# Optimization experiments

Measured on AMD Instinct MI355X. Metric: run time of the kernel, lower is better.

The kernel has to match this reference:

```python
import jax, jax.numpy as jnp
import numpy as np

GROUPS = 8
EPS = 1e-5
NUM_HEADS = 8


def group_norm(x, gamma, beta):
    # x: [B, C, N]; GroupNorm over (C//G, N) per group, per sample (torch semantics)
    B, C, N = x.shape
    xg = x.reshape(B, GROUPS, (C // GROUPS) * N)
    mean = xg.mean(axis=-1, keepdims=True)
    var = xg.var(axis=-1, keepdims=True)
    xn = ((xg - mean) * jax.lax.rsqrt(var + EPS)).reshape(B, C, N)
    return xn * gamma[None, :, None] + beta[None, :, None]


def setup_inputs() -> dict:
    key = jax.random.key(0)
    ks = jax.random.split(key, 6)
    B, N, C = 4, 2048, 512
    s = 0.02
    return {
        "x": jax.random.normal(ks[0], (B, N, C), jnp.float32),
        "pe": jax.random.normal(ks[1], (B, N, C), jnp.float32),
        "qkv_w": jax.random.normal(ks[2], (3 * C, C), jnp.float32) * s,
        "proj_w": jax.random.normal(ks[3], (C, C), jnp.float32) * s,
        "proj_b": jnp.zeros((C,), jnp.float32),
        "conv1_w": jax.random.normal(ks[4], (C, C), jnp.float32) * s,
        "conv1_b": jnp.zeros((C,), jnp.float32),
        "gn1_g": jnp.ones((C,), jnp.float32),
        "gn1_b": jnp.zeros((C,), jnp.float32),
        "conv2_w": jax.random.normal(ks[5], (C, C), jnp.float32) * s,
        "conv2_b": jnp.zeros((C,), jnp.float32),
        "gn2_g": jnp.ones((C,), jnp.float32),
        "gn2_b": jnp.zeros((C,), jnp.float32),
    }


def reference(x, pe, qkv_w, proj_w, proj_b, conv1_w, conv1_b, gn1_g, gn1_b,
              conv2_w, conv2_b, gn2_g, gn2_b):
    B, N, C = x.shape
    H = NUM_HEADS
    D = C // H
    scale = D ** -0.5

    pe_t = pe.transpose(0, 2, 1)  # [B, C, N]
    # Conv1d(kernel=1) == per-position linear over channels
    p1 = group_norm(jnp.einsum('oc,bcn->bon', conv1_w, pe_t) + conv1_b[None, :, None], gn1_g, gn1_b)
    p2 = group_norm(jnp.einsum('oc,bcn->bon', conv2_w, pe_t) + conv2_b[None, :, None], gn2_g, gn2_b)
    pe_1 = p1.transpose(0, 2, 1)                 # [B, N, C]
    pe_attn = jax.nn.sigmoid(jnp.einsum('bnc,bcm->bnm', pe_1, p2))  # [B, N, N]

    qkv = (x @ qkv_w.T).reshape(B, N, 3, H, D).transpose(2, 0, 3, 1, 4)  # [3, B, H, N, D]
    q, k, v = qkv[0], qkv[1], qkv[2]

    attn = jnp.einsum('bhnd,bhmd->bhnm', q, k) * scale
    attn = attn * pe_attn[:, None, :, :]
    attn = jax.nn.softmax(attn, axis=-1)

    out = jnp.einsum('bhnm,bhmd->bhnd', attn, v)          # [B, H, N, D]
    out = out.transpose(0, 2, 1, 3).reshape(B, N, C)
    return out @ proj_w.T + proj_b
```

## Files before the change

### kernel.cpp

```cpp
#include <hip/hip_runtime.h>
#include <hip/hip_bf16.h>

typedef __attribute__((ext_vector_type(8))) short bf16x8;
typedef __attribute__((ext_vector_type(4))) float f32x4;

__device__ __forceinline__ float bfu2f(unsigned int u) {
    return __uint_as_float(u << 16);
}
__device__ __forceinline__ unsigned short f2bfu(float f) {
    unsigned int u = __float_as_uint(f);
    u += 0x7fffu + ((u >> 16) & 1u);
    return (unsigned short)(u >> 16);
}

__global__ __launch_bounds__(256) void cvt2(const float* __restrict__ s0, unsigned short* __restrict__ d0,
                                            const float* __restrict__ s1, unsigned short* __restrict__ d1) {
    int i = blockIdx.x * 256 + threadIdx.x;
    const int stride = gridDim.x * 256;
    for (; i < 1048576; i += stride) {
        float4 v = reinterpret_cast<const float4*>(s0)[i];
        ushort4 o;
        o.x = f2bfu(v.x); o.y = f2bfu(v.y); o.z = f2bfu(v.z); o.w = f2bfu(v.w);
        reinterpret_cast<ushort4*>(d0)[i] = o;
        float4 u = reinterpret_cast<const float4*>(s1)[i];
        ushort4 p;
        p.x = f2bfu(u.x); p.y = f2bfu(u.y); p.z = f2bfu(u.z); p.w = f2bfu(u.w);
        reinterpret_cast<ushort4*>(d1)[i] = p;
    }
}

__global__ __launch_bounds__(256) void cvtw(const float* __restrict__ s0, unsigned short* __restrict__ d0,
                                            const float* __restrict__ s1, unsigned short* __restrict__ d1,
                                            const float* __restrict__ s2, unsigned short* __restrict__ d2,
                                            const float* __restrict__ s3, unsigned short* __restrict__ d3) {
    int i = blockIdx.x * 256 + threadIdx.x;
    const int stride = gridDim.x * 256;
    for (; i < 393216; i += stride) {
        const float* s; unsigned short* d; int j;
        if (i < 196608)      { s = s0; d = d0; j = i; }
        else if (i < 262144) { s = s1; d = d1; j = i - 196608; }
        else if (i < 327680) { s = s2; d = d2; j = i - 262144; }
        else                 { s = s3; d = d3; j = i - 327680; }
        float4 v = reinterpret_cast<const float4*>(s)[j];
        ushort4 o;
        o.x = f2bfu(v.x); o.y = f2bfu(v.y); o.z = f2bfu(v.z); o.w = f2bfu(v.w);
        reinterpret_cast<ushort4*>(d)[j] = o;
    }
}

template <int EPI>
__global__ __launch_bounds__(256) void gemm_nt(
    const unsigned short* __restrict__ A, const unsigned short* __restrict__ B,
    void* __restrict__ C0, void* __restrict__ C1, void* __restrict__ C2,
    const float* __restrict__ bias, int K, long sA, long sB, long sC) {
    __shared__ unsigned short As[128 * 40];
    __shared__ unsigned short Bs[128 * 40];
    const int tid = threadIdx.x;
    const int l = tid & 63, w = tid >> 6;
    const int wr = w >> 1, wc = w & 1, lr = l & 15, lh = l >> 4;
    const int m0 = blockIdx.y * 128, n0 = blockIdx.x * 128;
    A += (size_t)blockIdx.z * sA;
    B += (size_t)blockIdx.z * sB;
    f32x4 acc[4][4] = {};
    const int rowS = tid >> 2, partS = tid & 3;

    for (int k0 = 0; k0 < K; k0 += 32) {
        *reinterpret_cast<uint4*>(&As[rowS * 40 + partS * 8]) =
            *reinterpret_cast<const uint4*>(A + (size_t)(m0 + rowS) * K + k0 + partS * 8);
        *reinterpret_cast<uint4*>(&As[(rowS + 64) * 40 + partS * 8]) =
            *reinterpret_cast<const uint4*>(A + (size_t)(m0 + rowS + 64) * K + k0 + partS * 8);
        *reinterpret_cast<uint4*>(&Bs[rowS * 40 + partS * 8]) =
            *reinterpret_cast<const uint4*>(B + (size_t)(n0 + rowS) * K + k0 + partS * 8);
        *reinterpret_cast<uint4*>(&Bs[(rowS + 64) * 40 + partS * 8]) =
            *reinterpret_cast<const uint4*>(B + (size_t)(n0 + rowS + 64) * K + k0 + partS * 8);
        __syncthreads();
        bf16x8 af[4], bfr[4];
#pragma unroll
        for (int i = 0; i < 4; i++)
            af[i] = *reinterpret_cast<const bf16x8*>(&As[(wr * 64 + i * 16 + lr) * 40 + lh * 8]);
#pragma unroll
        for (int i = 0; i < 4; i++)
            bfr[i] = *reinterpret_cast<const bf16x8*>(&Bs[(wc * 64 + i * 16 + lr) * 40 + lh * 8]);
#pragma unroll
        for (int mi = 0; mi < 4; mi++)
#pragma unroll
            for (int ni = 0; ni < 4; ni++)
                acc[mi][ni] = __builtin_amdgcn_mfma_f32_16x16x32_bf16(af[mi], bfr[ni], acc[mi][ni], 0, 0, 0);
        __syncthreads();
    }

#pragma unroll
    for (int mi = 0; mi < 4; mi++) {
#pragma unroll
        for (int ni = 0; ni < 4; ni++) {
#pragma unroll
            for (int r = 0; r < 4; r++) {
                const int row = m0 + wr * 64 + mi * 16 + lh * 4 + r;
                const int col = n0 + wc * 64 + ni * 16 + lr;
                float v = acc[mi][ni][r];
                if constexpr (EPI == 0) {
                    v += bias[col];
                    ((unsigned short*)C0)[(size_t)row * 512 + col] = f2bfu(v);
                } else if constexpr (EPI == 1) {
                    const int part = col >> 9, hh = (col >> 6) & 7, d = col & 63;
                    const int b = row >> 11, n = row & 2047;
                    const size_t bh = (size_t)(b * 8 + hh);
                    if (part == 0)
                        ((unsigned short*)C0)[(bh * 2048 + n) * 64 + d] = f2bfu(v * 0.1803368801111244f);
                    else if (part == 1)
                        ((unsigned short*)C1)[(bh * 2048 + n) * 64 + d] = f2bfu(v);
                    else
                        ((unsigned short*)C2)[(bh * 64 + d) * 2048 + n] = f2bfu(v);
                } else if constexpr (EPI == 2) {
                    const float sg = 1.0f / (1.0f + __expf(-v));
                    ((unsigned short*)C0)[(size_t)blockIdx.z * sC + (size_t)row * 2048 + col] = f2bfu(sg);
                } else {
                    ((float*)C0)[(size_t)row * 512 + col] = v + bias[col];
                }
            }
        }
    }
}

__global__ __launch_bounds__(256) void gn_stats_part(const unsigned short* __restrict__ c1,
                                                     const unsigned short* __restrict__ c2,
                                                     float* __restrict__ part) {
    const int bgc = blockIdx.x;
    const int b = bgc >> 6, g = (bgc >> 3) & 7, ch = bgc & 7;
    const int tid = threadIdx.x;
    const size_t base = ((size_t)b * 2048 + ch * 256) * 512 + g * 64;
    float s1 = 0.f, q1 = 0.f, s2 = 0.f, q2 = 0.f;
    for (int c = tid; c < 2048; c += 256) {
        const int n = c >> 3, i8 = (c & 7) * 8;
        const size_t off = base + (size_t)n * 512 + i8;
        uint4 v1 = *reinterpret_cast<const uint4*>(c1 + off);
        uint4 v2 = *reinterpret_cast<const uint4*>(c2 + off);
        unsigned int a1[4] = {v1.x, v1.y, v1.z, v1.w};
        unsigned int a2[4] = {v2.x, v2.y, v2.z, v2.w};
#pragma unroll
        for (int j = 0; j < 4; j++) {
            float x0 = bfu2f(a1[j] & 0xffffu), x1 = bfu2f(a1[j] >> 16);
            s1 += x0 + x1; q1 += x0 * x0 + x1 * x1;
            float y0 = bfu2f(a2[j] & 0xffffu), y1 = bfu2f(a2[j] >> 16);
            s2 += y0 + y1; q2 += y0 * y0 + y1 * y1;
        }
    }
#pragma unroll
    for (int off = 32; off >= 1; off >>= 1) {
        s1 += __shfl_down(s1, off); q1 += __shfl_down(q1, off);
        s2 += __shfl_down(s2, off); q2 += __shfl_down(q2, off);
    }
    __shared__ float red[4][4];
    if ((tid & 63) == 0) {
        const int wv = tid >> 6;
        red[0][wv] = s1; red[1][wv] = q1; red[2][wv] = s2; red[3][wv] = q2;
    }
    __syncthreads();
    if (tid == 0) {
        part[bgc * 4 + 0] = red[0][0] + red[0][1] + red[0][2] + red[0][3];
        part[bgc * 4 + 1] = red[1][0] + red[1][1] + red[1][2] + red[1][3];
        part[bgc * 4 + 2] = red[2][0] + red[2][1] + red[2][2] + red[2][3];
        part[bgc * 4 + 3] = red[3][0] + red[3][1] + red[3][2] + red[3][3];
    }
}

__global__ __launch_bounds__(256) void gn_apply(unsigned short* __restrict__ c1,
                                                unsigned short* __restrict__ c2,
                                                const float* __restrict__ part,
                                                const float* __restrict__ g1, const float* __restrict__ b1,
                                                const float* __restrict__ g2, const float* __restrict__ b2) {
    __shared__ float sst[32][4];
    const int tid = threadIdx.x;
    if (tid < 32) {
        float S1 = 0.f, Q1 = 0.f, S2 = 0.f, Q2 = 0.f;
        for (int ch = 0; ch < 8; ch++) {
            const float* p = part + ((tid << 3) + ch) * 4;
            S1 += p[0]; Q1 += p[1]; S2 += p[2]; Q2 += p[3];
        }
        const float inv = 1.0f / 131072.0f;
        float m1 = S1 * inv, m2 = S2 * inv;
        float v1 = fmaxf(Q1 * inv - m1 * m1, 0.f);
        float v2 = fmaxf(Q2 * inv - m2 * m2, 0.f);
        sst[tid][0] = m1;
        sst[tid][1] = rsqrtf(v1 + 1e-5f);
        sst[tid][2] = m2;
        sst[tid][3] = rsqrtf(v2 + 1e-5f);
    }
    __syncthreads();
    int i = blockIdx.x * 256 + tid;
    const int stride = gridDim.x * 256;
    for (; i < 524288; i += stride) {
        const size_t e = (size_t)i * 8;
        const int b = (int)(e >> 20);
        const int o = (int)(e & 511);
        const int g = o >> 6;
        const float* st = sst[(b << 3) + g];
        const float m1 = st[0], r1 = st[1], m2 = st[2], r2 = st[3];
        uint4 v1 = *reinterpret_cast<const uint4*>(c1 + e);
        uint4 v2 = *reinterpret_cast<const uint4*>(c2 + e);
        unsigned int a1[4] = {v1.x, v1.y, v1.z, v1.w};
        unsigned int a2[4] = {v2.x, v2.y, v2.z, v2.w};
        unsigned int o1[4], o2[4];
#pragma unroll
        for (int j = 0; j < 4; j++) {
            const int oo = o + j * 2;
            float x0 = (bfu2f(a1[j] & 0xffffu) - m1) * r1 * g1[oo] + b1[oo];
            float x1 = (bfu2f(a1[j] >> 16) - m1) * r1 * g1[oo + 1] + b1[oo + 1];
            o1[j] = (unsigned int)f2bfu(x0) | ((unsigned int)f2bfu(x1) << 16);
            float y0 = (bfu2f(a2[j] & 0xffffu) - m2) * r2 * g2[oo] + b2[oo];
            float y1 = (bfu2f(a2[j] >> 16) - m2) * r2 * g2[oo + 1] + b2[oo + 1];
            o2[j] = (unsigned int)f2bfu(y0) | ((unsigned int)f2bfu(y1) << 16);
        }
        uint4 w1; w1.x = o1[0]; w1.y = o1[1]; w1.z = o1[2]; w1.w = o1[3];
        uint4 w2; w2.x = o2[0]; w2.y = o2[1]; w2.z = o2[2]; w2.w = o2[3];
        *reinterpret_cast<uint4*>(c1 + e) = w1;
        *reinterpret_cast<uint4*>(c2 + e) = w2;
    }
}

__global__ __launch_bounds__(256, 4) void attn_fused(
    const unsigned short* __restrict__ qb, const unsigned short* __restrict__ kb,
    const unsigned short* __restrict__ vT, const unsigned short* __restrict__ pea,
    unsigned short* __restrict__ hbuf) {
    __shared__ unsigned short Ks[2][64 * 64];
    __shared__ unsigned short Vs[2][64 * 64];
    const int tid = threadIdx.x, l = tid & 63, w = tid >> 6;
    const int lr = l & 15, lh = l >> 4;
    const int bid = blockIdx.x;
    const int h = bid >> 7, rst = bid & 127, nt = rst & 31, b = rst >> 5;
    const size_t bh = (size_t)(b * 8 + h);
    const unsigned short* qp = qb + bh * 2048 * 64;
    const unsigned short* kp = kb + bh * 2048 * 64;
    const unsigned short* vp = vT + bh * 64 * 2048;
    const unsigned short* pep = pea + (size_t)b * 2048 * 2048;
    const int n0 = nt * 64;

    bf16x8 qf[2];
    qf[0] = *reinterpret_cast<const bf16x8*>(qp + (size_t)(n0 + 16 * w + lr) * 64 + lh * 8);
    qf[1] = *reinterpret_cast<const bf16x8*>(qp + (size_t)(n0 + 16 * w + lr) * 64 + 32 + lh * 8);

    const int swz = (lr & 7) << 4;
    const int colK0 = ((16 * lh) ^ swz) >> 1;
    const int colK1 = ((64 + 16 * lh) ^ swz) >> 1;

    const unsigned short* perp = pep + (size_t)(n0 + 16 * w + lr) * 2048;
    uint2 peR[4];
#pragma unroll
    for (int mf = 0; mf < 4; mf++)
        peR[mf] = *reinterpret_cast<const uint2*>(perp + 16 * mf + 4 * lh);

    f32x4 oacc[4] = {};
    float mrun = -1e30f, lrun = 0.f;

    const int srow = l >> 3, sslot = l & 7;
    auto stage_kv = [&](int bufi, int m0) {
#pragma unroll
        for (int i = 0; i < 2; i++) {
            const int row = w * 16 + i * 8 + srow;
            const int cs = (sslot ^ (row & 7)) * 8;
            const int ldsoff = (w * 16 + i * 8) * 64;
            __builtin_amdgcn_global_load_lds(
                (const __attribute__((address_space(1))) void*)(kp + (size_t)(m0 + row) * 64 + cs),
                (__attribute__((address_space(3))) void*)&Ks[bufi][ldsoff], 16, 0, 0);
            __builtin_amdgcn_global_load_lds(
                (const __attribute__((address_space(1))) void*)(vp + (size_t)row * 2048 + m0 + cs),
                (__attribute__((address_space(3))) void*)&Vs[bufi][ldsoff], 16, 0, 0);
        }
    };

    stage_kv(0, 0);
    asm volatile("s_waitcnt vmcnt(0)" ::: "memory");
    __builtin_amdgcn_s_barrier();
    __builtin_amdgcn_sched_barrier(0);

    for (int mt = 0; mt < 32; mt++) {
        const int cur = mt & 1;
        if (mt + 1 < 32) stage_kv(cur ^ 1, (mt + 1) * 64);
        const unsigned short* Kb = Ks[cur];
        const unsigned short* Vb = Vs[cur];

        f32x4 st[4] = {};
        __builtin_amdgcn_s_setprio(1);
#pragma unroll
        for (int mf = 0; mf < 4; mf++) {
            bf16x8 kf0 = *reinterpret_cast<const bf16x8*>(&Kb[(mf * 16 + lr) * 64 + colK0]);
            bf16x8 kf1 = *reinterpret_cast<const bf16x8*>(&Kb[(mf * 16 + lr) * 64 + colK1]);
            st[mf] = __builtin_amdgcn_mfma_f32_16x16x32_bf16(kf0, qf[0], st[mf], 0, 0, 0);
            st[mf] = __builtin_amdgcn_mfma_f32_16x16x32_bf16(kf1, qf[1], st[mf], 0, 0, 0);
        }
        __builtin_amdgcn_s_setprio(0);
        asm volatile("s_waitcnt lgkmcnt(0)" ::: "memory");
        __builtin_amdgcn_s_barrier();
        __builtin_amdgcn_sched_barrier(0);

        float p[4][4];
#pragma unroll
        for (int mf = 0; mf < 4; mf++) {
            p[mf][0] = st[mf][0] * bfu2f(peR[mf].x & 0xffffu);
            p[mf][1] = st[mf][1] * bfu2f(peR[mf].x >> 16);
            p[mf][2] = st[mf][2] * bfu2f(peR[mf].y & 0xffffu);
            p[mf][3] = st[mf][3] * bfu2f(peR[mf].y >> 16);
        }
        uint2 peN[4];
        if (mt + 1 < 32) {
            const unsigned short* pn = perp + (mt + 1) * 64;
#pragma unroll
            for (int mf = 0; mf < 4; mf++)
                peN[mf] = *reinterpret_cast<const uint2*>(pn + 16 * mf + 4 * lh);
        }
        float pm = fmaxf(p[0][0], p[0][1]);
        pm = fmaxf(fmaxf(pm, p[0][2]), p[0][3]);
#pragma unroll
        for (int mf = 1; mf < 4; mf++) {
            pm = fmaxf(fmaxf(pm, p[mf][0]), p[mf][1]);
            pm = fmaxf(fmaxf(pm, p[mf][2]), p[mf][3]);
        }
        pm = fmaxf(pm, __shfl_xor(pm, 16));
        pm = fmaxf(pm, __shfl_xor(pm, 32));
        if (__any(pm > mrun + 11.5416f)) {
            const float mnew = fmaxf(mrun, pm);
            const float fac = __builtin_amdgcn_exp2f(mrun - mnew);
            lrun *= fac;
#pragma unroll
            for (int df = 0; df < 4; df++)
#pragma unroll
                for (int r = 0; r < 4; r++) oacc[df][r] *= fac;
            mrun = mnew;
        }
        float ss = 0.f;
        unsigned int pk[8];
#pragma unroll
        for (int mf = 0; mf < 4; mf++) {
#pragma unroll
            for (int t = 0; t < 2; t++) {
                const float a = __builtin_amdgcn_exp2f(p[mf][2 * t] - mrun);
                const float c = __builtin_amdgcn_exp2f(p[mf][2 * t + 1] - mrun);
                unsigned int pkv;
                asm("v_cvt_pk_bf16_f32 %0, %1, %2" : "=v"(pkv) : "v"(a), "v"(c));
                pk[mf * 2 + t] = pkv;
                ss += a + c;
            }
        }
        ss += __shfl_xor(ss, 16);
        ss += __shfl_xor(ss, 32);
        lrun += ss;
        unsigned short* PlW = &Ks[cur][w * 1024];
        const int plswz = (lr & 7) << 4;
#pragma unroll
        for (int mf = 0; mf < 4; mf++)
#pragma unroll
            for (int t = 0; t < 2; t++) {
                const int cb = (mf * 32 + lh * 8 + 4 * t) ^ plswz;
                *reinterpret_cast<unsigned int*>(&PlW[lr * 64 + (cb >> 1)]) = pk[mf * 2 + t];
            }
        bf16x8 pb0 = *reinterpret_cast<const bf16x8*>(&PlW[lr * 64 + (((lh * 16) ^ plswz) >> 1)]);
        bf16x8 pb1 = *reinterpret_cast<const bf16x8*>(&PlW[lr * 64 + (((64 + lh * 16) ^ plswz) >> 1)]);
        __builtin_amdgcn_s_setprio(1);
#pragma unroll
        for (int df = 0; df < 4; df++) {
            bf16x8 vf0 = *reinterpret_cast<const bf16x8*>(&Vb[(df * 16 + lr) * 64 + colK0]);
            bf16x8 vf1 = *reinterpret_cast<const bf16x8*>(&Vb[(df * 16 + lr) * 64 + colK1]);
            oacc[df] = __builtin_amdgcn_mfma_f32_16x16x32_bf16(vf0, pb0, oacc[df], 0, 0, 0);
            oacc[df] = __builtin_amdgcn_mfma_f32_16x16x32_bf16(vf1, pb1, oacc[df], 0, 0, 0);
        }
        __builtin_amdgcn_s_setprio(0);
        if (mt + 1 < 32) {
            asm volatile("s_waitcnt vmcnt(0) lgkmcnt(0)" ::: "memory");
            __builtin_amdgcn_s_barrier();
            __builtin_amdgcn_sched_barrier(0);
#pragma unroll
            for (int mf = 0; mf < 4; mf++) peR[mf] = peN[mf];
        }
    }
    const float inv = 1.0f / lrun;
    const size_t base = ((size_t)b * 2048 + n0 + 16 * w + lr) * 512 + h * 64;
#pragma unroll
    for (int df = 0; df < 4; df++) {
#pragma unroll
        for (int t = 0; t < 2; t++) {
            const unsigned int ua = f2bfu(oacc[df][2 * t] * inv);
            const unsigned int uc = f2bfu(oacc[df][2 * t + 1] * inv);
            *reinterpret_cast<unsigned int*>(&hbuf[base + 16 * df + 4 * lh + 2 * t]) = ua | (uc << 16);
        }
    }
}

extern "C" void kernel_launch(void* const* d_in, const int* in_sizes, int n_in,
                              void* d_out, int out_size, void* d_ws, size_t ws_size,
                              hipStream_t stream) {
    const float* x       = (const float*)d_in[0];
    const float* pe      = (const float*)d_in[1];
    const float* qkv_w   = (const float*)d_in[2];
    const float* proj_w  = (const float*)d_in[3];
    const float* proj_b  = (const float*)d_in[4];
    const float* conv1_w = (const float*)d_in[5];
    const float* conv1_b = (const float*)d_in[6];
    const float* gn1_g   = (const float*)d_in[7];
    const float* gn1_b   = (const float*)d_in[8];
    const float* conv2_w = (const float*)d_in[9];
    const float* conv2_b = (const float*)d_in[10];
    const float* gn2_g   = (const float*)d_in[11];
    const float* gn2_b   = (const float*)d_in[12];
    float* out = (float*)d_out;

    char* ws = (char*)d_ws;
    size_t off = 0;
    auto alloc = [&](size_t bytes) -> void* {
        void* p = ws + off;
        off += (bytes + 255) & ~(size_t)255;
        return p;
    };
    unsigned short* xb     = (unsigned short*)alloc(8388608);
    unsigned short* peb    = (unsigned short*)alloc(8388608);
    unsigned short* qkvwb  = (unsigned short*)alloc(1572864);
    unsigned short* projwb = (unsigned short*)alloc(524288);
    unsigned short* w1b    = (unsigned short*)alloc(524288);
    unsigned short* w2b    = (unsigned short*)alloc(524288);
    unsigned short* c1b    = (unsigned short*)alloc(8388608);
    unsigned short* c2b    = (unsigned short*)alloc(8388608);
    unsigned short* qbuf   = (unsigned short*)alloc(8388608);
    unsigned short* kbuf   = (unsigned short*)alloc(8388608);
    unsigned short* vtb    = (unsigned short*)alloc(8388608);
    unsigned short* peatt  = (unsigned short*)alloc(33554432);
    unsigned short* hbuf   = (unsigned short*)alloc(8388608);
    float* part            = (float*)alloc(4096);

    dim3 blk(256);
    cvt2<<<1024, blk, 0, stream>>>(x, xb, pe, peb);
    cvtw<<<512, blk, 0, stream>>>(qkv_w, qkvwb, proj_w, projwb, conv1_w, w1b, conv2_w, w2b);

    gemm_nt<0><<<dim3(4, 64, 1), blk, 0, stream>>>(peb, w1b, c1b, nullptr, nullptr, conv1_b, 512, 0, 0, 0);
    gemm_nt<0><<<dim3(4, 64, 1), blk, 0, stream>>>(peb, w2b, c2b, nullptr, nullptr, conv2_b, 512, 0, 0, 0);
    gn_stats_part<<<256, blk, 0, stream>>>(c1b, c2b, part);
    gn_apply<<<1024, blk, 0, stream>>>(c1b, c2b, part, gn1_g, gn1_b, gn2_g, gn2_b);
    gemm_nt<1><<<dim3(12, 64, 1), blk, 0, stream>>>(xb, qkvwb, qbuf, kbuf, vtb, nullptr, 512, 0, 0, 0);
    gemm_nt<2><<<dim3(16, 16, 4), blk, 0, stream>>>(c1b, c2b, peatt, nullptr, nullptr, nullptr, 512,
                                                    1048576, 1048576, 4194304);
    attn_fused<<<dim3(1024, 1, 1), blk, 0, stream>>>(qbuf, kbuf, vtb, peatt, hbuf);
    gemm_nt<3><<<dim3(4, 64, 1), blk, 0, stream>>>(hbuf, projwb, out, nullptr, nullptr, proj_b, 512, 0, 0, 0);
}
```

Before: 250.4 us.

## Double-buffer GEMM tiles via direct global-to-LDS loads; give attention its own P buffer

The GEMM main loop now uses two LDS buffers filled with global_load_lds direct-to-LDS transfers and an XOR swizzle instead of padded rows. The next K tile is prefetched while MFMAs run on the current one, with a single barrier per step and raised wave priority around the MFMAs. In the attention kernel, the per-wave P tile moves from the reused K buffer to a dedicated LDS array, which removes a mid-iteration barrier. The cost is extra LDS per block, which may reduce occupancy, plus reliance on the correctness of the swizzled layout.

After: 232.5 us. 1.08x faster.

```diff
diff --git a/kernel.cpp b/kernel.cpp
--- a/kernel.cpp
+++ b/kernel.cpp
@@ -53,8 +53,8 @@
     const unsigned short* __restrict__ A, const unsigned short* __restrict__ B,
     void* __restrict__ C0, void* __restrict__ C1, void* __restrict__ C2,
     const float* __restrict__ bias, int K, long sA, long sB, long sC) {
-    __shared__ unsigned short As[128 * 40];
-    __shared__ unsigned short Bs[128 * 40];
+    __shared__ unsigned short As[2][128 * 32];
+    __shared__ unsigned short Bs[2][128 * 32];
     const int tid = threadIdx.x;
     const int l = tid & 63, w = tid >> 6;
     const int wr = w >> 1, wc = w & 1, lr = l & 15, lh = l >> 4;
@@ -62,31 +62,52 @@
     A += (size_t)blockIdx.z * sA;
     B += (size_t)blockIdx.z * sB;
     f32x4 acc[4][4] = {};
-    const int rowS = tid >> 2, partS = tid & 3;
-
-    for (int k0 = 0; k0 < K; k0 += 32) {
-        *reinterpret_cast<uint4*>(&As[rowS * 40 + partS * 8]) =
-            *reinterpret_cast<const uint4*>(A + (size_t)(m0 + rowS) * K + k0 + partS * 8);
-        *reinterpret_cast<uint4*>(&As[(rowS + 64) * 40 + partS * 8]) =
-            *reinterpret_cast<const uint4*>(A + (size_t)(m0 + rowS + 64) * K + k0 + partS * 8);
-        *reinterpret_cast<uint4*>(&Bs[rowS * 40 + partS * 8]) =
-            *reinterpret_cast<const uint4*>(B + (size_t)(n0 + rowS) * K + k0 + partS * 8);
-        *reinterpret_cast<uint4*>(&Bs[(rowS + 64) * 40 + partS * 8]) =
-            *reinterpret_cast<const uint4*>(B + (size_t)(n0 + rowS + 64) * K + k0 + partS * 8);
-        __syncthreads();
+
+    const int srow = l >> 2, sslot = l & 3;
+    auto stage = [&](int bufi, int k0) {
+#pragma unroll
+        for (int i = 0; i < 2; i++) {
+            const int row = w * 32 + i * 16 + srow;
+            const int cs = (sslot ^ (row & 3)) * 8;
+            const int ldsoff = (w * 32 + i * 16) * 32;
+            __builtin_amdgcn_global_load_lds(
+                (const __attribute__((address_space(1))) void*)(A + (size_t)(m0 + row) * K + k0 + cs),
+                (__attribute__((address_space(3))) void*)&As[bufi][ldsoff], 16, 0, 0);
+            __builtin_amdgcn_global_load_lds(
+                (const __attribute__((address_space(1))) void*)(B + (size_t)(n0 + row) * K + k0 + cs),
+                (__attribute__((address_space(3))) void*)&Bs[bufi][ldsoff], 16, 0, 0);
+        }
+    };
+
+    const int nks = K >> 5;
+    stage(0, 0);
+    asm volatile("s_waitcnt vmcnt(0)" ::: "memory");
+    __builtin_amdgcn_s_barrier();
+    __builtin_amdgcn_sched_barrier(0);
+
+    const int colA = (lh ^ (lr & 3)) << 3;
+    for (int ks = 0; ks < nks; ks++) {
+        const int cur = ks & 1;
+        if (ks + 1 < nks) stage(cur ^ 1, (ks + 1) << 5);
         bf16x8 af[4], bfr[4];
 #pragma unroll
         for (int i = 0; i < 4; i++)
-            af[i] = *reinterpret_cast<const bf16x8*>(&As[(wr * 64 + i * 16 + lr) * 40 + lh * 8]);
+            af[i] = *reinterpret_cast<const bf16x8*>(&As[cur][(wr * 64 + i * 16 + lr) * 32 + colA]);
 #pragma unroll
         for (int i = 0; i < 4; i++)
-            bfr[i] = *reinterpret_cast<const bf16x8*>(&Bs[(wc * 64 + i * 16 + lr) * 40 + lh * 8]);
+            bfr[i] = *reinterpret_cast<const bf16x8*>(&Bs[cur][(wc * 64 + i * 16 + lr) * 32 + colA]);
+        __builtin_amdgcn_s_setprio(1);
 #pragma unroll
         for (int mi = 0; mi < 4; mi++)
 #pragma unroll
             for (int ni = 0; ni < 4; ni++)
                 acc[mi][ni] = __builtin_amdgcn_mfma_f32_16x16x32_bf16(af[mi], bfr[ni], acc[mi][ni], 0, 0, 0);
-        __syncthreads();
+        __builtin_amdgcn_s_setprio(0);
+        if (ks + 1 < nks) {
+            asm volatile("s_waitcnt vmcnt(0) lgkmcnt(0)" ::: "memory");
+            __builtin_amdgcn_s_barrier();
+            __builtin_amdgcn_sched_barrier(0);
+        }
     }
 
 #pragma unroll
@@ -224,6 +245,7 @@
     unsigned short* __restrict__ hbuf) {
     __shared__ unsigned short Ks[2][64 * 64];
     __shared__ unsigned short Vs[2][64 * 64];
+    __shared__ unsigned short Pl[4][16 * 64];
     const int tid = threadIdx.x, l = tid & 63, w = tid >> 6;
     const int lr = l & 15, lh = l >> 4;
     const int bid = blockIdx.x;
@@ -289,9 +311,6 @@
             st[mf] = __builtin_amdgcn_mfma_f32_16x16x32_bf16(kf1, qf[1], st[mf], 0, 0, 0);
         }
         __builtin_amdgcn_s_setprio(0);
-        asm volatile("s_waitcnt lgkmcnt(0)" ::: "memory");
-        __builtin_amdgcn_s_barrier();
-        __builtin_amdgcn_sched_barrier(0);
 
         float p[4][4];
 #pragma unroll
@@ -344,7 +363,7 @@
         ss += __shfl_xor(ss, 16);
         ss += __shfl_xor(ss, 32);
         lrun += ss;
-        unsigned short* PlW = &Ks[cur][w * 1024];
+        unsigned short* PlW = Pl[w];
         const int plswz = (lr & 7) << 4;
 #pragma unroll
         for (int mf = 0; mf < 4; mf++)
```
